# Optimization experiments

Measured on AMD Instinct MI355X. Metric: run time of the kernel, lower is better.

## Reference

```python
import jax, jax.numpy as jnp
import numpy as np

# Mesh/packing dims: deltaV_packed.view(B, M, V, ndims) requires N = B*M*V
B, M, V = 2, 4, 40000
N = B * M * V            # 320_000 packed vertices
E = 960000               # ~3 edges per vertex (triangle mesh)
F_IN = 128               # n_input_features
LAT = 128                # latent_channels
NDIMS = 3
N_HIDDEN = 2             # n_f2f_hidden_layer


def graph_conv(x, edges, W0, b0, W1, b1):
    """pytorch3d-style GraphConv: w0(x) + sum_{j in N(i)} w1(x_j), undirected edges."""
    h0 = x @ W0 + b0                     # self term  [N, out]
    h1 = x @ W1 + b1                     # neighbor messages [N, out]
    src, dst = edges[:, 0], edges[:, 1]
    agg = jnp.zeros_like(h0).at[src].add(h1[dst]).at[dst].add(h1[src])
    return h0 + agg


def setup_inputs() -> dict:
    key = jax.random.key(0)
    ks = jax.random.split(key, 20)
    inp = {
        "features": jax.random.normal(ks[0], (N, F_IN), jnp.float32),
        "edges": jax.random.randint(ks[1], (E, 2), 0, N, dtype=jnp.int32),
    }
    # Layer dims: f2f first (F_IN->LAT), 2 hidden (LAT->LAT), f2v (LAT->NDIMS).
    dims = [(F_IN, LAT), (LAT, LAT), (LAT, LAT), (LAT, NDIMS)]
    for i, (din, dout) in enumerate(dims):
        kk = jax.random.split(ks[2 + i], 4)
        s = 1.0 / np.sqrt(din)
        inp[f"W0_{i}"] = jax.random.normal(kk[0], (din, dout), jnp.float32) * s
        inp[f"b0_{i}"] = jnp.zeros((dout,), jnp.float32)
        inp[f"W1_{i}"] = jax.random.normal(kk[1], (din, dout), jnp.float32) * s
        inp[f"b1_{i}"] = jnp.zeros((dout,), jnp.float32)
    return inp


def reference(features, edges,
              W0_0, b0_0, W1_0, b1_0,
              W0_1, b0_1, W1_1, b1_1,
              W0_2, b0_2, W1_2, b1_2,
              W0_3, b0_3, W1_3, b1_3):
    # Features2FeaturesResidual: first GC + 2 hidden GCs (ReLU each, norm='none'),
    # residual skip (identity since F_IN == LAT).
    h = jax.nn.relu(graph_conv(features, edges, W0_0, b0_0, W1_0, b1_0))
    h = jax.nn.relu(graph_conv(h, edges, W0_1, b0_1, W1_1, b1_1))
    h = jax.nn.relu(graph_conv(h, edges, W0_2, b0_2, W1_2, b1_2))
    h = h + features
    # f2v: GC(latent -> ndims), no activation
    deltaV = graph_conv(h, edges, W0_3, b0_3, W1_3, b1_3)
    return deltaV.reshape(B, M, V, NDIMS)
```

## Files before the change

kernel.cpp:

```cpp
#include <hip/hip_runtime.h>
#include <hip/hip_bf16.h>

#define NNODES 320000
#define NEDGES 960000

typedef __attribute__((ext_vector_type(8))) short short8;
typedef __attribute__((ext_vector_type(4))) float f32x4;

__device__ __forceinline__ float b2f(unsigned short u) {
    return __uint_as_float(((unsigned)u) << 16);
}
__device__ __forceinline__ unsigned short f2b(float f) {
    __hip_bfloat16 h = __float2bfloat16(f);
    union { __hip_bfloat16 h; unsigned short u; } cv;
    cv.h = h;
    return cv.u;
}


__global__ void k_zero(int* p, int n) {
    int i = blockIdx.x * blockDim.x + threadIdx.x;
    int s = gridDim.x * blockDim.x;
    for (; i < n; i += s) p[i] = 0;
}

__global__ void k_count(const int* __restrict__ edges, int* __restrict__ deg) {
    int i = blockIdx.x * blockDim.x + threadIdx.x;
    int s = gridDim.x * blockDim.x;
    for (; i < NEDGES; i += s) {
        int a = edges[2 * i], b = edges[2 * i + 1];
        atomicAdd(&deg[a], 1);
        atomicAdd(&deg[b], 1);
    }
}

#define SCAN_BLOCK 256
#define SCAN_ITEMS 8
#define SCAN_CHUNK 2048
#define SCAN_NB 157

__global__ void k_scan1(const int* __restrict__ deg, int* __restrict__ bsum) {
    __shared__ int sd[SCAN_BLOCK];
    int b = blockIdx.x, t = threadIdx.x;
    int base = b * SCAN_CHUNK + t * SCAN_ITEMS;
    int s = 0;
    for (int i = 0; i < SCAN_ITEMS; i++) {
        int g = base + i;
        if (g < NNODES) s += deg[g];
    }
    sd[t] = s;
    __syncthreads();
    for (int off = 128; off > 0; off >>= 1) {
        if (t < off) sd[t] += sd[t + off];
        __syncthreads();
    }
    if (t == 0) bsum[b] = sd[0];
}

__global__ void k_scan2(int* bsum, int* rowptr) {
    if (blockIdx.x == 0 && threadIdx.x == 0) {
        int run = 0;
        for (int b = 0; b < SCAN_NB; b++) {
            int v = bsum[b];
            bsum[b] = run;
            run += v;
        }
        rowptr[NNODES] = run;
    }
}

__global__ void k_scan3(int* __restrict__ deg_cursor, int* __restrict__ rowptr,
                        const int* __restrict__ bsum) {
    __shared__ int sd[SCAN_BLOCK];
    int b = blockIdx.x, t = threadIdx.x;
    int base = b * SCAN_CHUNK + t * SCAN_ITEMS;
    int v[SCAN_ITEMS];
    int s = 0;
    for (int i = 0; i < SCAN_ITEMS; i++) {
        int g = base + i;
        v[i] = (g < NNODES) ? deg_cursor[g] : 0;
        s += v[i];
    }
    sd[t] = s;
    __syncthreads();
    for (int off = 1; off < SCAN_BLOCK; off <<= 1) {
        int x = (t >= off) ? sd[t - off] : 0;
        __syncthreads();
        sd[t] += x;
        __syncthreads();
    }
    int prefix = bsum[b] + (sd[t] - s);
    for (int i = 0; i < SCAN_ITEMS; i++) {
        int g = base + i;
        if (g < NNODES) {
            rowptr[g] = prefix;
            deg_cursor[g] = prefix;
            prefix += v[i];
        }
    }
}

__global__ void k_fill(const int* __restrict__ edges, int* __restrict__ cursor,
                       int* __restrict__ adj) {
    int i = blockIdx.x * blockDim.x + threadIdx.x;
    int s = gridDim.x * blockDim.x;
    for (; i < NEDGES; i += s) {
        int a = edges[2 * i], b = edges[2 * i + 1];
        adj[atomicAdd(&cursor[a], 1)] = b;
        adj[atomicAdd(&cursor[b], 1)] = a;
    }
}


#define LDK 136

__global__ __launch_bounds__(256) void k_gemm(
    const void* __restrict__ xin, int xIsF32,
    const float* __restrict__ W0p, const float* __restrict__ W1p,
    const float* __restrict__ b0p, const float* __restrict__ b1p,
    unsigned short* __restrict__ h01) {
    __shared__ __align__(16) unsigned short Wt[128 * LDK];
    __shared__ __align__(16) unsigned short At[64 * LDK];
    __shared__ float biasS[128];

    int tid = threadIdx.x;
    int half = blockIdx.x & 1;
    const float* W = half ? W1p : W0p;
    const float* bb = half ? b1p : b0p;

    for (int it = 0; it < 64; ++it) {
        int idx = it * 256 + tid;
        int c = idx & 127;
        int k = idx >> 7;
        Wt[c * LDK + k] = f2b(W[k * 128 + c]);
    }
    if (tid < 128) biasS[tid] = bb[tid];

    int wave = tid >> 6, lane = tid & 63;
    int wm = wave >> 1, wn = wave & 1;
    int nchunks = gridDim.x >> 1;

    for (int rt = blockIdx.x >> 1; rt < NNODES / 64; rt += nchunks) {
        __syncthreads();
        int rowBase = rt * 64;
        if (xIsF32) {
            const float* xf = (const float*)xin;
            for (int it = 0; it < 8; ++it) {
                int e = (it * 256 + tid) * 4;
                int r = e >> 7;
                int k = e & 127;
                float4 v = *(const float4*)&xf[(size_t)(rowBase + r) * 128 + k];
                unsigned short* dst = &At[r * LDK + k];
                dst[0] = f2b(v.x);
                dst[1] = f2b(v.y);
                dst[2] = f2b(v.z);
                dst[3] = f2b(v.w);
            }
        } else {
            const unsigned short* xb = (const unsigned short*)xin;
            for (int it = 0; it < 4; ++it) {
                int e = (it * 256 + tid) * 8;
                int r = e >> 7;
                int k = e & 127;
                *(uint4*)&At[r * LDK + k] =
                    *(const uint4*)&xb[(size_t)(rowBase + r) * 128 + k];
            }
        }
        __syncthreads();

        f32x4 acc[2][4];
        for (int i = 0; i < 2; i++)
            for (int j = 0; j < 4; j++) acc[i][j] = (f32x4){0.f, 0.f, 0.f, 0.f};

        for (int ks = 0; ks < 4; ++ks) {
            int kk = ks * 32 + ((lane >> 4) << 3);
            short8 aF[2], bF[4];
            for (int mf = 0; mf < 2; ++mf) {
                int r = wm * 32 + mf * 16 + (lane & 15);
                aF[mf] = *(const short8*)&At[r * LDK + kk];
            }
            for (int nf = 0; nf < 4; ++nf) {
                int c = wn * 64 + nf * 16 + (lane & 15);
                bF[nf] = *(const short8*)&Wt[c * LDK + kk];
            }
            for (int mf = 0; mf < 2; mf++)
                for (int nf = 0; nf < 4; nf++)
                    acc[mf][nf] = __builtin_amdgcn_mfma_f32_16x16x32_bf16(
                        aF[mf], bF[nf], acc[mf][nf], 0, 0, 0);
        }

        for (int mf = 0; mf < 2; mf++)
            for (int nf = 0; nf < 4; nf++) {
                int r0 = rowBase + wm * 32 + mf * 16 + ((lane >> 4) << 2);
                int cl = wn * 64 + nf * 16 + (lane & 15);
                int c = half * 128 + cl;
                float bv = biasS[cl];
                f32x4 d = acc[mf][nf];
                for (int q = 0; q < 4; q++)
                    h01[(size_t)(r0 + q) * 256 + c] = f2b(d[q] + bv);
            }
    }
}


template <int MODE>
__global__ void k_agg(const unsigned short* __restrict__ h01,
                      const int* __restrict__ rowptr, const int* __restrict__ adj,
                      const float* __restrict__ features,
                      unsigned short* __restrict__ act) {
    int wid = (blockIdx.x * blockDim.x + threadIdx.x) >> 6;
    int lane = threadIdx.x & 63;
    int nw = (gridDim.x * blockDim.x) >> 6;
    for (int node = wid; node < NNODES; node += nw) {
        unsigned u = *(const unsigned*)&h01[(size_t)node * 256 + lane * 2];
        float a0 = b2f(u & 0xffff), a1 = b2f(u >> 16);
        int s = rowptr[node], e = rowptr[node + 1];
        int p = s;
        for (; p + 2 <= e; p += 2) {
            int j0 = adj[p], j1 = adj[p + 1];
            unsigned v0 = *(const unsigned*)&h01[(size_t)j0 * 256 + 128 + lane * 2];
            unsigned v1 = *(const unsigned*)&h01[(size_t)j1 * 256 + 128 + lane * 2];
            a0 += b2f(v0 & 0xffff) + b2f(v1 & 0xffff);
            a1 += b2f(v0 >> 16) + b2f(v1 >> 16);
        }
        if (p < e) {
            int j = adj[p];
            unsigned v = *(const unsigned*)&h01[(size_t)j * 256 + 128 + lane * 2];
            a0 += b2f(v & 0xffff);
            a1 += b2f(v >> 16);
        }
        a0 = fmaxf(a0, 0.f);
        a1 = fmaxf(a1, 0.f);
        if (MODE == 2) {
            float2 f = *(const float2*)&features[(size_t)node * 128 + lane * 2];
            a0 += f.x;
            a1 += f.y;
        }
        unsigned out = (unsigned)f2b(a0) | ((unsigned)f2b(a1) << 16);
        *(unsigned*)&act[(size_t)node * 128 + lane * 2] = out;
    }
}


#define LDK3 136

__global__ __launch_bounds__(256) void k_gemm3(
    const unsigned short* __restrict__ act, const float* __restrict__ W0p,
    const float* __restrict__ W1p, const float* __restrict__ b0p,
    const float* __restrict__ b1p, float* __restrict__ h3) {
    __shared__ __align__(16) unsigned short xs[128 * LDK3];
    __shared__ float Ws[128 * 8];
    __shared__ float bs[8];
    int tid = threadIdx.x;
    int nodeBase = blockIdx.x * 128;

    for (int idx = tid; idx < 384; idx += 256) {
        int k = idx / 3, c = idx - k * 3;
        Ws[k * 8 + c] = W0p[idx];
        Ws[k * 8 + 4 + c] = W1p[idx];
    }
    if (tid < 3) {
        bs[tid] = b0p[tid];
        bs[4 + tid] = b1p[tid];
    }
    for (int it = 0; it < 8; ++it) {
        int e = (it * 256 + tid) * 8;
        int r = e >> 7;
        int k = e & 127;
        *(uint4*)&xs[r * LDK3 + k] = *(const uint4*)&act[(size_t)(nodeBase + r) * 128 + k];
    }
    __syncthreads();

    int n = tid >> 1, half = tid & 1;
    float a0 = 0.f, a1 = 0.f, a2 = 0.f;
    for (int k0 = 0; k0 < 128; k0 += 8) {
        uint4 v = *(const uint4*)&xs[n * LDK3 + k0];
        unsigned vv[4] = {v.x, v.y, v.z, v.w};
#pragma unroll
        for (int q = 0; q < 4; q++) {
            int k = k0 + 2 * q;
            float x0 = b2f(vv[q] & 0xffff), x1 = b2f(vv[q] >> 16);
            const float* w = &Ws[k * 8 + half * 4];
            a0 += x0 * w[0] + x1 * w[8];
            a1 += x0 * w[1] + x1 * w[9];
            a2 += x0 * w[2] + x1 * w[10];
        }
    }
    float* dst = &h3[(size_t)(nodeBase + n) * 8 + half * 4];
    dst[0] = a0 + bs[half * 4 + 0];
    dst[1] = a1 + bs[half * 4 + 1];
    dst[2] = a2 + bs[half * 4 + 2];
}

__global__ void k_agg3(const float* __restrict__ h3, const int* __restrict__ rowptr,
                       const int* __restrict__ adj, float* __restrict__ out) {
    int i = blockIdx.x * blockDim.x + threadIdx.x;
    int stride = gridDim.x * blockDim.x;
    for (int node = i; node < NNODES; node += stride) {
        float a0 = h3[(size_t)node * 8 + 0];
        float a1 = h3[(size_t)node * 8 + 1];
        float a2 = h3[(size_t)node * 8 + 2];
        int s = rowptr[node], e = rowptr[node + 1];
        for (int p = s; p < e; ++p) {
            int j = adj[p];
            float4 v = *(const float4*)&h3[(size_t)j * 8 + 4];
            a0 += v.x;
            a1 += v.y;
            a2 += v.z;
        }
        out[(size_t)node * 3 + 0] = a0;
        out[(size_t)node * 3 + 1] = a1;
        out[(size_t)node * 3 + 2] = a2;
    }
}


extern "C" void kernel_launch(void* const* d_in, const int* in_sizes, int n_in,
                              void* d_out, int out_size, void* d_ws, size_t ws_size,
                              hipStream_t stream) {
    const float* features = (const float*)d_in[0];
    const int* edges = (const int*)d_in[1];
    const float *W0[4], *B0[4], *W1[4], *B1[4];
    for (int i = 0; i < 4; i++) {
        W0[i] = (const float*)d_in[2 + 4 * i];
        B0[i] = (const float*)d_in[3 + 4 * i];
        W1[i] = (const float*)d_in[4 + 4 * i];
        B1[i] = (const float*)d_in[5 + 4 * i];
    }

    char* p = (char*)d_ws;
    auto alloc = [&](size_t bytes) {
        void* r = (void*)p;
        p += (bytes + 255) & ~(size_t)255;
        return r;
    };
    int* rowptr = (int*)alloc((NNODES + 1) * sizeof(int));
    int* cursor = (int*)alloc((NNODES + 1) * sizeof(int));
    int* adj = (int*)alloc((size_t)2 * NEDGES * sizeof(int));
    int* bsum = (int*)alloc(1024);
    unsigned short* h01 = (unsigned short*)alloc((size_t)NNODES * 256 * 2);
    unsigned short* actb = (unsigned short*)alloc((size_t)NNODES * 128 * 2);
    float* h3 = (float*)h01;

    k_zero<<<1024, 256, 0, stream>>>(cursor, NNODES + 1);
    k_count<<<2048, 256, 0, stream>>>(edges, cursor);
    k_scan1<<<SCAN_NB, SCAN_BLOCK, 0, stream>>>(cursor, bsum);
    k_scan2<<<1, 64, 0, stream>>>(bsum, rowptr);
    k_scan3<<<SCAN_NB, SCAN_BLOCK, 0, stream>>>(cursor, rowptr, bsum);
    k_fill<<<2048, 256, 0, stream>>>(edges, cursor, adj);

    k_gemm<<<2048, 256, 0, stream>>>(features, 1, W0[0], W1[0], B0[0], B1[0], h01);
    k_agg<0><<<16384, 256, 0, stream>>>(h01, rowptr, adj, nullptr, actb);
    k_gemm<<<2048, 256, 0, stream>>>(actb, 0, W0[1], W1[1], B0[1], B1[1], h01);
    k_agg<0><<<16384, 256, 0, stream>>>(h01, rowptr, adj, nullptr, actb);
    k_gemm<<<2048, 256, 0, stream>>>(actb, 0, W0[2], W1[2], B0[2], B1[2], h01);
    k_agg<2><<<16384, 256, 0, stream>>>(h01, rowptr, adj, features, actb);
    k_gemm3<<<NNODES / 128, 256, 0, stream>>>(actb, W0[3], W1[3], B0[3], B1[3], h3);
    k_agg3<<<2048, 256, 0, stream>>>(h3, rowptr, adj, (float*)d_out);
}
```

Baseline: 1.203 ms.

## Aggregate inputs before GEMM and fuse self/neighbor terms into one K=256 MFMA

Uses linearity to reorder each graph conv: first gather and sum neighbor inputs (bf16, 128 wide), then run one GEMM over the concatenated [x, sum_x] with stacked [W0; W1] weights. The bias b1 is scaled by the node degree, and ReLU and the residual are fused into the GEMM epilogue. This halves the gather width versus gathering the 256-wide h01, drops the h01 intermediate and its write/read, and keeps weights in registers after a one-time bf16 conversion. It adds a gather pass per layer and extra bf16 rounding of the summed inputs, which could change accuracy.

```diff
diff --git a/kernel.cpp b/kernel.cpp
--- a/kernel.cpp
+++ b/kernel.cpp
@@ -70,7 +70,7 @@
 }
 
 __global__ void k_scan3(int* __restrict__ deg_cursor, int* __restrict__ rowptr,
-                        const int* __restrict__ bsum) {
+                        const int* __restrict__ bsum, float* __restrict__ degf) {
     __shared__ int sd[SCAN_BLOCK];
     int b = blockIdx.x, t = threadIdx.x;
     int base = b * SCAN_CHUNK + t * SCAN_ITEMS;
@@ -95,6 +95,7 @@
         if (g < NNODES) {
             rowptr[g] = prefix;
             deg_cursor[g] = prefix;
+            degf[g] = (float)v[i];
             prefix += v[i];
         }
     }
@@ -112,205 +113,202 @@
 }
 
 
-#define LDK 136
-
-__global__ __launch_bounds__(256) void k_gemm(
-    const void* __restrict__ xin, int xIsF32,
-    const float* __restrict__ W0p, const float* __restrict__ W1p,
-    const float* __restrict__ b0p, const float* __restrict__ b1p,
-    unsigned short* __restrict__ h01) {
-    __shared__ __align__(16) unsigned short Wt[128 * LDK];
-    __shared__ __align__(16) unsigned short At[64 * LDK];
-    __shared__ float biasS[128];
-
-    int tid = threadIdx.x;
-    int half = blockIdx.x & 1;
-    const float* W = half ? W1p : W0p;
-    const float* bb = half ? b1p : b0p;
-
-    for (int it = 0; it < 64; ++it) {
-        int idx = it * 256 + tid;
-        int c = idx & 127;
-        int k = idx >> 7;
-        Wt[c * LDK + k] = f2b(W[k * 128 + c]);
-    }
-    if (tid < 128) biasS[tid] = bb[tid];
-
-    int wave = tid >> 6, lane = tid & 63;
-    int wm = wave >> 1, wn = wave & 1;
-    int nchunks = gridDim.x >> 1;
-
-    for (int rt = blockIdx.x >> 1; rt < NNODES / 64; rt += nchunks) {
-        __syncthreads();
-        int rowBase = rt * 64;
-        if (xIsF32) {
-            const float* xf = (const float*)xin;
-            for (int it = 0; it < 8; ++it) {
-                int e = (it * 256 + tid) * 4;
-                int r = e >> 7;
-                int k = e & 127;
-                float4 v = *(const float4*)&xf[(size_t)(rowBase + r) * 128 + k];
-                unsigned short* dst = &At[r * LDK + k];
-                dst[0] = f2b(v.x);
-                dst[1] = f2b(v.y);
-                dst[2] = f2b(v.z);
-                dst[3] = f2b(v.w);
-            }
-        } else {
-            const unsigned short* xb = (const unsigned short*)xin;
-            for (int it = 0; it < 4; ++it) {
-                int e = (it * 256 + tid) * 8;
-                int r = e >> 7;
-                int k = e & 127;
-                *(uint4*)&At[r * LDK + k] =
-                    *(const uint4*)&xb[(size_t)(rowBase + r) * 128 + k];
-            }
-        }
-        __syncthreads();
-
-        f32x4 acc[2][4];
-        for (int i = 0; i < 2; i++)
-            for (int j = 0; j < 4; j++) acc[i][j] = (f32x4){0.f, 0.f, 0.f, 0.f};
-
-        for (int ks = 0; ks < 4; ++ks) {
-            int kk = ks * 32 + ((lane >> 4) << 3);
-            short8 aF[2], bF[4];
-            for (int mf = 0; mf < 2; ++mf) {
-                int r = wm * 32 + mf * 16 + (lane & 15);
-                aF[mf] = *(const short8*)&At[r * LDK + kk];
-            }
-            for (int nf = 0; nf < 4; ++nf) {
-                int c = wn * 64 + nf * 16 + (lane & 15);
-                bF[nf] = *(const short8*)&Wt[c * LDK + kk];
-            }
-            for (int mf = 0; mf < 2; mf++)
-                for (int nf = 0; nf < 4; nf++)
-                    acc[mf][nf] = __builtin_amdgcn_mfma_f32_16x16x32_bf16(
-                        aF[mf], bF[nf], acc[mf][nf], 0, 0, 0);
-        }
-
-        for (int mf = 0; mf < 2; mf++)
-            for (int nf = 0; nf < 4; nf++) {
-                int r0 = rowBase + wm * 32 + mf * 16 + ((lane >> 4) << 2);
-                int cl = wn * 64 + nf * 16 + (lane & 15);
-                int c = half * 128 + cl;
-                float bv = biasS[cl];
-                f32x4 d = acc[mf][nf];
-                for (int q = 0; q < 4; q++)
-                    h01[(size_t)(r0 + q) * 256 + c] = f2b(d[q] + bv);
-            }
-    }
-}
-
-
-template <int MODE>
-__global__ void k_agg(const unsigned short* __restrict__ h01,
-                      const int* __restrict__ rowptr, const int* __restrict__ adj,
-                      const float* __restrict__ features,
-                      unsigned short* __restrict__ act) {
+__global__ void k_cvt(const float* __restrict__ f, unsigned short* __restrict__ o,
+                      long n4) {
+    long i = (long)blockIdx.x * blockDim.x + threadIdx.x;
+    long s = (long)gridDim.x * blockDim.x;
+    for (; i < n4; i += s) {
+        float4 v = *(const float4*)&f[i * 4];
+        uint2 u;
+        u.x = (unsigned)f2b(v.x) | ((unsigned)f2b(v.y) << 16);
+        u.y = (unsigned)f2b(v.z) | ((unsigned)f2b(v.w) << 16);
+        *(uint2*)&o[i * 4] = u;
+    }
+}
+
+__global__ void k_cvtW(const float* __restrict__ W0, const float* __restrict__ W1,
+                       unsigned short* __restrict__ Wt) {
+    int idx = blockIdx.x * blockDim.x + threadIdx.x;
+    if (idx >= 128 * 256) return;
+    int c = idx >> 8, k = idx & 255;
+    float v = (k < 128) ? W0[k * 128 + c] : W1[(k - 128) * 128 + c];
+    Wt[idx] = f2b(v);
+}
+
+
+__global__ __launch_bounds__(256) void k_gather(
+    const unsigned short* __restrict__ x, const int* __restrict__ rowptr,
+    const int* __restrict__ adj, unsigned short* __restrict__ xsum) {
     int wid = (blockIdx.x * blockDim.x + threadIdx.x) >> 6;
     int lane = threadIdx.x & 63;
     int nw = (gridDim.x * blockDim.x) >> 6;
     for (int node = wid; node < NNODES; node += nw) {
-        unsigned u = *(const unsigned*)&h01[(size_t)node * 256 + lane * 2];
-        float a0 = b2f(u & 0xffff), a1 = b2f(u >> 16);
         int s = rowptr[node], e = rowptr[node + 1];
-        int p = s;
-        for (; p + 2 <= e; p += 2) {
-            int j0 = adj[p], j1 = adj[p + 1];
-            unsigned v0 = *(const unsigned*)&h01[(size_t)j0 * 256 + 128 + lane * 2];
-            unsigned v1 = *(const unsigned*)&h01[(size_t)j1 * 256 + 128 + lane * 2];
-            a0 += b2f(v0 & 0xffff) + b2f(v1 & 0xffff);
-            a1 += b2f(v0 >> 16) + b2f(v1 >> 16);
-        }
-        if (p < e) {
-            int j = adj[p];
-            unsigned v = *(const unsigned*)&h01[(size_t)j * 256 + 128 + lane * 2];
-            a0 += b2f(v & 0xffff);
-            a1 += b2f(v >> 16);
-        }
-        a0 = fmaxf(a0, 0.f);
-        a1 = fmaxf(a1, 0.f);
-        if (MODE == 2) {
-            float2 f = *(const float2*)&features[(size_t)node * 128 + lane * 2];
-            a0 += f.x;
-            a1 += f.y;
-        }
-        unsigned out = (unsigned)f2b(a0) | ((unsigned)f2b(a1) << 16);
-        *(unsigned*)&act[(size_t)node * 128 + lane * 2] = out;
-    }
-}
-
-
-#define LDK3 136
-
-__global__ __launch_bounds__(256) void k_gemm3(
-    const unsigned short* __restrict__ act, const float* __restrict__ W0p,
-    const float* __restrict__ W1p, const float* __restrict__ b0p,
-    const float* __restrict__ b1p, float* __restrict__ h3) {
-    __shared__ __align__(16) unsigned short xs[128 * LDK3];
-    __shared__ float Ws[128 * 8];
-    __shared__ float bs[8];
+        float a0 = 0.f, a1 = 0.f;
+        for (int p = s; p < e; p += 8) {
+            int cnt = e - p;
+            if (cnt > 8) cnt = 8;
+            int jv = (lane < cnt) ? adj[p + lane] : 0;
+            unsigned vbuf[8];
+#pragma unroll
+            for (int q = 0; q < 8; ++q) {
+                int j = __shfl(jv, q, 64);
+                vbuf[q] = (q < cnt)
+                              ? *(const unsigned*)&x[(size_t)j * 128 + lane * 2]
+                              : 0u;
+            }
+#pragma unroll
+            for (int q = 0; q < 8; ++q) {
+                a0 += b2f(vbuf[q] & 0xffff);
+                a1 += b2f(vbuf[q] >> 16);
+            }
+        }
+        unsigned o = (unsigned)f2b(a0) | ((unsigned)f2b(a1) << 16);
+        *(unsigned*)&xsum[(size_t)node * 128 + lane * 2] = o;
+    }
+}
+
+
+#define XLD 136
+
+template <int RES>
+__global__ __launch_bounds__(256) void k_gemmF(
+    const unsigned short* x, const unsigned short* __restrict__ xsum,
+    const unsigned short* __restrict__ Wt, const float* __restrict__ b0,
+    const float* __restrict__ b1, const float* __restrict__ degf,
+    const unsigned short* __restrict__ feat, unsigned short* out) {
+    __shared__ __align__(16) unsigned short Xs[64 * XLD];
+    __shared__ __align__(16) unsigned short Ss[64 * XLD];
+
     int tid = threadIdx.x;
-    int nodeBase = blockIdx.x * 128;
+    int wave = tid >> 6, lane = tid & 63;
+    int wm = wave >> 1, wn = wave & 1;
+    int kg = (lane >> 4) << 3;
+    int cl = lane & 15;
+
+    short8 bF[8][4];
+#pragma unroll
+    for (int ks = 0; ks < 8; ++ks)
+#pragma unroll
+        for (int nf = 0; nf < 4; ++nf) {
+            int c = wn * 64 + nf * 16 + cl;
+            bF[ks][nf] = *(const short8*)&Wt[(size_t)c * 256 + ks * 32 + kg];
+        }
+
+    int rowBase = blockIdx.x * 64;
+#pragma unroll
+    for (int it = 0; it < 4; ++it) {
+        int e = (it * 256 + tid) * 8;
+        int r = e >> 7, k = e & 127;
+        *(uint4*)&Xs[r * XLD + k] = *(const uint4*)&x[(size_t)(rowBase + r) * 128 + k];
+        *(uint4*)&Ss[r * XLD + k] =
+            *(const uint4*)&xsum[(size_t)(rowBase + r) * 128 + k];
+    }
+    __syncthreads();
+
+    f32x4 acc[2][4];
+#pragma unroll
+    for (int i = 0; i < 2; i++)
+#pragma unroll
+        for (int j = 0; j < 4; j++) acc[i][j] = (f32x4){0.f, 0.f, 0.f, 0.f};
+
+#pragma unroll
+    for (int ks = 0; ks < 8; ++ks) {
+        const unsigned short* src = (ks < 4) ? Xs : Ss;
+        int kk = (ks & 3) * 32 + kg;
+        short8 aF[2];
+#pragma unroll
+        for (int mf = 0; mf < 2; ++mf) {
+            int r = wm * 32 + mf * 16 + cl;
+            aF[mf] = *(const short8*)&src[r * XLD + kk];
+        }
+#pragma unroll
+        for (int mf = 0; mf < 2; mf++)
+#pragma unroll
+            for (int nf = 0; nf < 4; nf++)
+                acc[mf][nf] = __builtin_amdgcn_mfma_f32_16x16x32_bf16(
+                    aF[mf], bF[ks][nf], acc[mf][nf], 0, 0, 0);
+    }
+
+#pragma unroll
+    for (int nf = 0; nf < 4; nf++) {
+        int c = wn * 64 + nf * 16 + cl;
+        float bias0 = b0[c], bias1 = b1[c];
+#pragma unroll
+        for (int mf = 0; mf < 2; mf++) {
+            int r0 = rowBase + wm * 32 + mf * 16 + ((lane >> 4) << 2);
+            f32x4 d = acc[mf][nf];
+#pragma unroll
+            for (int q = 0; q < 4; q++) {
+                int r = r0 + q;
+                float v = d[q] + bias0 + degf[r] * bias1;
+                v = fmaxf(v, 0.f);
+                if (RES) v += b2f(feat[(size_t)r * 128 + c]);
+                out[(size_t)r * 128 + c] = f2b(v);
+            }
+        }
+    }
+}
+
+
+__global__ __launch_bounds__(256) void k_fin(
+    const unsigned short* __restrict__ act, const unsigned short* __restrict__ hsum,
+    const float* __restrict__ W0, const float* __restrict__ W1,
+    const float* __restrict__ b0, const float* __restrict__ b1,
+    const float* __restrict__ degf, float* __restrict__ out) {
+    __shared__ __align__(16) unsigned short xa[64 * XLD];
+    __shared__ __align__(16) unsigned short xs2[64 * XLD];
+    __shared__ float Wf[768];
+    __shared__ float ps[64][4][4];
+
+    int tid = threadIdx.x;
+    int nodeBase = blockIdx.x * 64;
 
     for (int idx = tid; idx < 384; idx += 256) {
-        int k = idx / 3, c = idx - k * 3;
-        Ws[k * 8 + c] = W0p[idx];
-        Ws[k * 8 + 4 + c] = W1p[idx];
-    }
-    if (tid < 3) {
-        bs[tid] = b0p[tid];
-        bs[4 + tid] = b1p[tid];
-    }
-    for (int it = 0; it < 8; ++it) {
+        Wf[idx] = W0[idx];
+        Wf[384 + idx] = W1[idx];
+    }
+#pragma unroll
+    for (int it = 0; it < 4; ++it) {
         int e = (it * 256 + tid) * 8;
-        int r = e >> 7;
-        int k = e & 127;
-        *(uint4*)&xs[r * LDK3 + k] = *(const uint4*)&act[(size_t)(nodeBase + r) * 128 + k];
-    }
-    __syncthreads();
-
-    int n = tid >> 1, half = tid & 1;
+        int r = e >> 7, k = e & 127;
+        *(uint4*)&xa[r * XLD + k] = *(const uint4*)&act[(size_t)(nodeBase + r) * 128 + k];
+        *(uint4*)&xs2[r * XLD + k] =
+            *(const uint4*)&hsum[(size_t)(nodeBase + r) * 128 + k];
+    }
+    __syncthreads();
+
+    int n = tid >> 2, q = tid & 3;
+    const unsigned short* src = (q < 2) ? xa : xs2;
+    int kloc = (q & 1) * 64;
     float a0 = 0.f, a1 = 0.f, a2 = 0.f;
-    for (int k0 = 0; k0 < 128; k0 += 8) {
-        uint4 v = *(const uint4*)&xs[n * LDK3 + k0];
+#pragma unroll
+    for (int kk = 0; kk < 64; kk += 8) {
+        uint4 v = *(const uint4*)&src[n * XLD + kloc + kk];
         unsigned vv[4] = {v.x, v.y, v.z, v.w};
 #pragma unroll
-        for (int q = 0; q < 4; q++) {
-            int k = k0 + 2 * q;
-            float x0 = b2f(vv[q] & 0xffff), x1 = b2f(vv[q] >> 16);
-            const float* w = &Ws[k * 8 + half * 4];
-            a0 += x0 * w[0] + x1 * w[8];
-            a1 += x0 * w[1] + x1 * w[9];
-            a2 += x0 * w[2] + x1 * w[10];
-        }
-    }
-    float* dst = &h3[(size_t)(nodeBase + n) * 8 + half * 4];
-    dst[0] = a0 + bs[half * 4 + 0];
-    dst[1] = a1 + bs[half * 4 + 1];
-    dst[2] = a2 + bs[half * 4 + 2];
-}
-
-__global__ void k_agg3(const float* __restrict__ h3, const int* __restrict__ rowptr,
-                       const int* __restrict__ adj, float* __restrict__ out) {
-    int i = blockIdx.x * blockDim.x + threadIdx.x;
-    int stride = gridDim.x * blockDim.x;
-    for (int node = i; node < NNODES; node += stride) {
-        float a0 = h3[(size_t)node * 8 + 0];
-        float a1 = h3[(size_t)node * 8 + 1];
-        float a2 = h3[(size_t)node * 8 + 2];
-        int s = rowptr[node], e = rowptr[node + 1];
-        for (int p = s; p < e; ++p) {
-            int j = adj[p];
-            float4 v = *(const float4*)&h3[(size_t)j * 8 + 4];
-            a0 += v.x;
-            a1 += v.y;
-            a2 += v.z;
-        }
-        out[(size_t)node * 3 + 0] = a0;
-        out[(size_t)node * 3 + 1] = a1;
-        out[(size_t)node * 3 + 2] = a2;
+        for (int t = 0; t < 4; t++) {
+            int kgl = q * 64 + kk + 2 * t;
+            float x0 = b2f(vv[t] & 0xffff), x1 = b2f(vv[t] >> 16);
+            const float* w = &Wf[kgl * 3];
+            a0 += x0 * w[0] + x1 * w[3];
+            a1 += x0 * w[1] + x1 * w[4];
+            a2 += x0 * w[2] + x1 * w[5];
+        }
+    }
+    ps[n][q][0] = a0;
+    ps[n][q][1] = a1;
+    ps[n][q][2] = a2;
+    __syncthreads();
+    if (q == 0) {
+        int node = nodeBase + n;
+        float dg = degf[node];
+#pragma unroll
+        for (int c = 0; c < 3; c++) {
+            float d = ps[n][0][c] + ps[n][1][c] + ps[n][2][c] + ps[n][3][c] +
+                      b0[c] + dg * b1[c];
+            out[(size_t)node * 3 + c] = d;
+        }
     }
 }
 
@@ -336,25 +334,35 @@
     };
     int* rowptr = (int*)alloc((NNODES + 1) * sizeof(int));
     int* cursor = (int*)alloc((NNODES + 1) * sizeof(int));
+    float* degf = (float*)alloc(NNODES * sizeof(float));
     int* adj = (int*)alloc((size_t)2 * NEDGES * sizeof(int));
     int* bsum = (int*)alloc(1024);
-    unsigned short* h01 = (unsigned short*)alloc((size_t)NNODES * 256 * 2);
-    unsigned short* actb = (unsigned short*)alloc((size_t)NNODES * 128 * 2);
-    float* h3 = (float*)h01;
+    unsigned short* feat_bf = (unsigned short*)alloc((size_t)NNODES * 128 * 2);
+    unsigned short* act = (unsigned short*)alloc((size_t)NNODES * 128 * 2);
+    unsigned short* xsum = (unsigned short*)alloc((size_t)NNODES * 128 * 2);
+    unsigned short* Wtb = (unsigned short*)alloc((size_t)3 * 128 * 256 * 2);
 
     k_zero<<<1024, 256, 0, stream>>>(cursor, NNODES + 1);
     k_count<<<2048, 256, 0, stream>>>(edges, cursor);
     k_scan1<<<SCAN_NB, SCAN_BLOCK, 0, stream>>>(cursor, bsum);
     k_scan2<<<1, 64, 0, stream>>>(bsum, rowptr);
-    k_scan3<<<SCAN_NB, SCAN_BLOCK, 0, stream>>>(cursor, rowptr, bsum);
+    k_scan3<<<SCAN_NB, SCAN_BLOCK, 0, stream>>>(cursor, rowptr, bsum, degf);
     k_fill<<<2048, 256, 0, stream>>>(edges, cursor, adj);
 
-    k_gemm<<<2048, 256, 0, stream>>>(features, 1, W0[0], W1[0], B0[0], B1[0], h01);
-    k_agg<0><<<16384, 256, 0, stream>>>(h01, rowptr, adj, nullptr, actb);
-    k_gemm<<<2048, 256, 0, stream>>>(actb, 0, W0[1], W1[1], B0[1], B1[1], h01);
-    k_agg<0><<<16384, 256, 0, stream>>>(h01, rowptr, adj, nullptr, actb);
-    k_gemm<<<2048, 256, 0, stream>>>(actb, 0, W0[2], W1[2], B0[2], B1[2], h01);
-    k_agg<2><<<16384, 256, 0, stream>>>(h01, rowptr, adj, features, actb);
-    k_gemm3<<<NNODES / 128, 256, 0, stream>>>(actb, W0[3], W1[3], B0[3], B1[3], h3);
-    k_agg3<<<2048, 256, 0, stream>>>(h3, rowptr, adj, (float*)d_out);
-}
+    k_cvt<<<2048, 256, 0, stream>>>(features, feat_bf, (long)NNODES * 128 / 4);
+    for (int l = 0; l < 3; l++)
+        k_cvtW<<<128, 256, 0, stream>>>(W0[l], W1[l], Wtb + (size_t)l * 128 * 256);
+
+    k_gather<<<8192, 256, 0, stream>>>(feat_bf, rowptr, adj, xsum);
+    k_gemmF<0><<<NNODES / 64, 256, 0, stream>>>(feat_bf, xsum, Wtb, B0[0], B1[0],
+                                                degf, nullptr, act);
+    k_gather<<<8192, 256, 0, stream>>>(act, rowptr, adj, xsum);
+    k_gemmF<0><<<NNODES / 64, 256, 0, stream>>>(act, xsum, Wtb + 128 * 256, B0[1],
+                                                B1[1], degf, nullptr, act);
+    k_gather<<<8192, 256, 0, stream>>>(act, rowptr, adj, xsum);
+    k_gemmF<1><<<NNODES / 64, 256, 0, stream>>>(act, xsum, Wtb + 2 * 128 * 256,
+                                                B0[2], B1[2], degf, feat_bf, act);
+    k_gather<<<8192, 256, 0, stream>>>(act, rowptr, adj, xsum);
+    k_fin<<<NNODES / 64, 256, 0, stream>>>(act, xsum, W0[3], W1[3], B0[3], B1[3],
+                                           degf, (float*)d_out);
+}
```

Result: no change. 1.209 ms (+0.5%).
